# Kernel optimization log

Measured on AMD Instinct MI355X. Metric: run time of the kernel, lower is better.

## Reference

```python
import math
import jax, jax.numpy as jnp
import numpy as np

D_IN, R_S, T_MAX = 1024, 256, 2048
B, T = 8, 2048


def setup_inputs() -> dict:
    key = jax.random.key(0)
    ks = jax.random.split(key, 8)
    u = jax.random.normal(ks[0], (B, T, D_IN), dtype=jnp.float32)
    h0_r = jax.random.normal(ks[1], (B, R_S), dtype=jnp.float32)
    h0_i = jax.random.normal(ks[2], (B, R_S), dtype=jnp.float32)
    # parameters (lambda_raw randomized instead of zeros so sigmoid is nontrivial)
    lambda_raw = jax.random.normal(ks[3], (R_S,), dtype=jnp.float32)
    # omega init exactly as in the torch module
    log_min, log_max = math.log(1.0 / T_MAX), math.log(math.pi)
    n = np.arange(1, R_S + 1, dtype=np.float32)
    weyl_freqs = n * math.pi / R_S
    log_freqs = np.exp(np.linspace(log_min, log_max, R_S, dtype=np.float32))
    omega = jnp.asarray(0.5 * weyl_freqs + 0.5 * log_freqs, dtype=jnp.float32)
    W_proj = jax.random.normal(ks[4], (R_S, D_IN), dtype=jnp.float32) / math.sqrt(D_IN)
    W_res = jax.random.normal(ks[5], (2 * R_S, D_IN), dtype=jnp.float32) / math.sqrt(D_IN)
    ln_gamma = jnp.ones((2 * R_S,), dtype=jnp.float32)
    ln_beta = jnp.zeros((2 * R_S,), dtype=jnp.float32)
    return {"u": u, "h0_r": h0_r, "h0_i": h0_i, "lambda_raw": lambda_raw,
            "omega": omega, "W_proj": W_proj, "W_res": W_res,
            "ln_gamma": ln_gamma, "ln_beta": ln_beta}


def _layernorm(x, gamma, beta, eps=1e-5):
    mu = jnp.mean(x, axis=-1, keepdims=True)
    var = jnp.mean(jnp.square(x - mu), axis=-1, keepdims=True)
    return (x - mu) * jax.lax.rsqrt(var + eps) * gamma + beta


def reference(u, h0_r, h0_i, lambda_raw, omega, W_proj, W_res, ln_gamma, ln_beta):
    Bb, Tt, _ = u.shape
    lam = -jax.nn.sigmoid(lambda_raw) * 5.0                      # [R]
    t = jnp.arange(Tt, dtype=jnp.float32)                        # [T]
    decay = jnp.exp(lam[:, None] * t[None, :])                   # [R,T]
    phase = omega[:, None] * t[None, :]                          # [R,T]
    f_r = decay * jnp.cos(phase)
    f_i = decay * jnp.sin(phase)
    u_proj = jnp.einsum('btd,rd->brt', u, W_proj)                # [B,R,T]
    n_fft = 2 * Tt
    U_f = jnp.fft.rfft(u_proj, n=n_fft, axis=-1)                 # [B,R,F]
    F_r = jnp.fft.rfft(f_r, n=n_fft, axis=-1)[None]              # [1,R,F]
    F_i = jnp.fft.rfft(f_i, n=n_fft, axis=-1)[None]
    h_r = jnp.fft.irfft(U_f * F_r, n=n_fft, axis=-1)[..., :Tt]   # [B,R,T]
    h_i = jnp.fft.irfft(U_f * F_i, n=n_fft, axis=-1)[..., :Tt]
    # ZIR correction from initial state
    t_zir = t + 1.0
    decay_z = jnp.exp(lam[:, None] * t_zir[None, :])             # [R,T]
    phase_z = omega[:, None] * t_zir[None, :]
    f_r_z = decay_z * jnp.cos(phase_z)
    f_i_z = decay_z * jnp.sin(phase_z)
    h0r = h0_r[:, :, None]                                       # [B,R,1]
    h0i = h0_i[:, :, None]
    h_r = h_r + h0r * f_r_z[None] - h0i * f_i_z[None]
    h_i = h_i + h0r * f_i_z[None] + h0i * f_r_z[None]
    h_r = jnp.swapaxes(h_r, 1, 2)                                # [B,T,R]
    h_i = jnp.swapaxes(h_i, 1, 2)
    ssm_out = jnp.concatenate([h_r, h_i], axis=-1)               # [B,T,2R]
    res = jnp.einsum('btd,ed->bte', u, W_res)                    # [B,T,2R]
    out = _layernorm(ssm_out + res, ln_gamma, ln_beta)
    final_r = jax.lax.stop_gradient(h_r[:, -1])
    final_i = jax.lax.stop_gradient(h_i[:, -1])
    return out, final_r, final_i
```

## Files before the change

### kernel.cpp

```cpp
#include <hip/hip_runtime.h>
#include <math.h>

#define T_LEN 2048
#define BB    8
#define RS    256
#define DIN   1024
#define NE    768
#define M_TOT (BB * T_LEN)
#define LCH   32
#define NCH   (T_LEN / LCH)
#define OUT_MAIN (M_TOT * 512)

typedef unsigned short ushort;
typedef unsigned int   uint;
typedef short  short8  __attribute__((ext_vector_type(8)));
typedef float  f32x4   __attribute__((ext_vector_type(4)));
typedef ushort ushort8 __attribute__((ext_vector_type(8)));

__device__ __forceinline__ ushort f2bf_rn(float x) {
    uint u = __float_as_uint(x);
    return (ushort)((u + 0x7FFFu + ((u >> 16) & 1u)) >> 16);
}
__device__ __forceinline__ float bf2f(ushort b) {
    return __uint_as_float(((uint)b) << 16);
}

__device__ __forceinline__ void gload16(const ushort* g, ushort* l) {
    __builtin_amdgcn_global_load_lds(
        (const __attribute__((address_space(1))) uint*)g,
        (__attribute__((address_space(3))) uint*)l, 16, 0, 0);
}

__global__ __launch_bounds__(256) void split_kernel(
    const float* __restrict__ src, ushort* __restrict__ hi,
    ushort* __restrict__ lo, int n8)
{
    int i = blockIdx.x * blockDim.x + threadIdx.x;
    const int stride = gridDim.x * blockDim.x;
    for (; i < n8; i += stride) {
        const float4 x0 = ((const float4*)src)[(size_t)i * 2 + 0];
        const float4 x1 = ((const float4*)src)[(size_t)i * 2 + 1];
        const float xs[8] = {x0.x, x0.y, x0.z, x0.w, x1.x, x1.y, x1.z, x1.w};
        ushort8 hv, lv;
#pragma unroll
        for (int j = 0; j < 8; ++j) {
            const ushort hb = f2bf_rn(xs[j]);
            hv[j] = hb;
            lv[j] = f2bf_rn(xs[j] - bf2f(hb));
        }
        ((ushort8*)hi)[i] = hv;
        ((ushort8*)lo)[i] = lv;
    }
}

#define Bb 128
#define BK 32

__global__ __launch_bounds__(256) void gemm_mfma(
    const ushort* __restrict__ Uh, const ushort* __restrict__ Ul,
    const ushort* __restrict__ Wh, const ushort* __restrict__ Wl,
    float* __restrict__ C)
{
    __shared__ ushort Ah[Bb * BK], Al[Bb * BK], Bh[Bb * BK], Bl[Bb * BK];
    const int tid  = threadIdx.x;
    const int bn   = blockIdx.x;
    const int bm   = blockIdx.y;
    const int wid  = tid >> 6;
    const int lane = tid & 63;
    const int wr   = wid >> 1, wc = wid & 1;
    const int fr   = lane & 15;
    const int fq   = lane >> 4;

    const int srow = tid >> 2;
    const int skk  = (tid & 3) * 8;
    const ushort* gAh = Uh + (size_t)(bm * 128 + srow) * DIN + skk;
    const ushort* gAl = Ul + (size_t)(bm * 128 + srow) * DIN + skk;
    const ushort* gBh = Wh + (size_t)(bn * 128 + srow) * DIN + skk;
    const ushort* gBl = Wl + (size_t)(bn * 128 + srow) * DIN + skk;
    ushort* lAh0 = Ah + tid * 8; ushort* lAh1 = Ah + 64 * BK + tid * 8;
    ushort* lAl0 = Al + tid * 8; ushort* lAl1 = Al + 64 * BK + tid * 8;
    ushort* lBh0 = Bh + tid * 8; ushort* lBh1 = Bh + 64 * BK + tid * 8;
    ushort* lBl0 = Bl + tid * 8; ushort* lBl1 = Bl + 64 * BK + tid * 8;
    const size_t rstep = (size_t)64 * DIN;

    f32x4 acc[4][4];
#pragma unroll
    for (int m = 0; m < 4; ++m)
#pragma unroll
        for (int n = 0; n < 4; ++n) acc[m][n] = (f32x4){0.f, 0.f, 0.f, 0.f};

    for (int kk = 0; kk < DIN; kk += BK) {
        gload16(gAh + kk, lAh0); gload16(gAh + kk + rstep, lAh1);
        gload16(gAl + kk, lAl0); gload16(gAl + kk + rstep, lAl1);
        gload16(gBh + kk, lBh0); gload16(gBh + kk + rstep, lBh1);
        gload16(gBl + kk, lBl0); gload16(gBl + kk + rstep, lBl1);
        __syncthreads();

        short8 ah[4], al[4], bh[4], bl[4];
#pragma unroll
        for (int m = 0; m < 4; ++m) {
            const int row = wr * 64 + m * 16 + fr;
            ah[m] = *(const short8*)&Ah[row * BK + fq * 8];
            al[m] = *(const short8*)&Al[row * BK + fq * 8];
        }
#pragma unroll
        for (int n = 0; n < 4; ++n) {
            const int col = wc * 64 + n * 16 + fr;
            bh[n] = *(const short8*)&Bh[col * BK + fq * 8];
            bl[n] = *(const short8*)&Bl[col * BK + fq * 8];
        }
#pragma unroll
        for (int m = 0; m < 4; ++m)
#pragma unroll
            for (int n = 0; n < 4; ++n) {
                acc[m][n] = __builtin_amdgcn_mfma_f32_16x16x32_bf16(ah[m], bh[n], acc[m][n], 0, 0, 0);
                acc[m][n] = __builtin_amdgcn_mfma_f32_16x16x32_bf16(ah[m], bl[n], acc[m][n], 0, 0, 0);
                acc[m][n] = __builtin_amdgcn_mfma_f32_16x16x32_bf16(al[m], bh[n], acc[m][n], 0, 0, 0);
            }
        __syncthreads();
    }

    const int crow0 = bm * 128 + wr * 64;
    const int ccol0 = bn * 128 + wc * 64;
#pragma unroll
    for (int m = 0; m < 4; ++m) {
        const int row = crow0 + m * 16 + fq * 4;
#pragma unroll
        for (int n = 0; n < 4; ++n) {
            const int col = ccol0 + n * 16 + fr;
#pragma unroll
            for (int j = 0; j < 4; ++j)
                C[(size_t)(row + j) * NE + col] = acc[m][n][j];
        }
    }
}

__device__ inline void pole(const float* __restrict__ lraw, const float* __restrict__ om,
                            int r, float& zr, float& zi, float& lam, float& o)
{
    const float x   = lraw[r];
    const float sig = 1.f / (1.f + expf(-x));
    lam = -5.f * sig;
    o   = om[r];
    const float er = expf(lam);
    zr = er * cosf(o);
    zi = er * sinf(o);
}

__global__ __launch_bounds__(256) void carry_kernel(
    const float* __restrict__ C, const float* __restrict__ lraw,
    const float* __restrict__ om, float2* __restrict__ carry)
{
    const int c = blockIdx.x, b = blockIdx.y, r = threadIdx.x;
    __shared__ float tile[LCH][RS];
    const int m0 = b * T_LEN + c * LCH;
    for (int s = 0; s < LCH; ++s)
        tile[s][r] = C[(size_t)(m0 + s) * NE + r];
    float zr, zi, lam, o;
    pole(lraw, om, r, zr, zi, lam, o);
    __syncthreads();
    float hr = 0.f, hi = 0.f;
#pragma unroll 4
    for (int s = 0; s < LCH; ++s) {
        const float u  = tile[s][r];
        const float nr = zr * hr - zi * hi + u;
        const float ni = zr * hi + zi * hr;
        hr = nr; hi = ni;
    }
    carry[(size_t)(b * NCH + c) * RS + r] = make_float2(hr, hi);
}

__global__ __launch_bounds__(256) void chunk_scan_kernel(
    const float2* __restrict__ carry, const float* __restrict__ h0r,
    const float* __restrict__ h0i, const float* __restrict__ lraw,
    const float* __restrict__ om, float2* __restrict__ S, float* __restrict__ out)
{
    const int b = blockIdx.x, r = threadIdx.x;
    float zr, zi, lam, o;
    pole(lraw, om, r, zr, zi, lam, o);
    const float eL  = expf(lam * (float)LCH);
    const float zLr = eL * cosf(o * (float)LCH);
    const float zLi = eL * sinf(o * (float)LCH);
    float sr = h0r[b * RS + r];
    float si = h0i[b * RS + r];
    for (int c = 0; c < NCH; ++c) {
        S[(size_t)(b * NCH + c) * RS + r] = make_float2(sr, si);
        const float2 cc = carry[(size_t)(b * NCH + c) * RS + r];
        const float nr = zLr * sr - zLi * si + cc.x;
        const float ni = zLr * si + zLi * sr + cc.y;
        sr = nr; si = ni;
    }
    out[OUT_MAIN + b * RS + r]            = sr;
    out[OUT_MAIN + BB * RS + b * RS + r]  = si;
}

__global__ __launch_bounds__(256) void scan_ln_kernel(
    const float* __restrict__ C, const float2* __restrict__ S,
    const float* __restrict__ lraw, const float* __restrict__ om,
    const float* __restrict__ gamma, const float* __restrict__ beta,
    float* __restrict__ out)
{
    const int c = blockIdx.x, b = blockIdx.y, r = threadIdx.x;
    __shared__ float tile[LCH][RS];
    __shared__ float redA[4], redB[4];
    const int m0 = b * T_LEN + c * LCH;
    for (int s = 0; s < LCH; ++s)
        tile[s][r] = C[(size_t)(m0 + s) * NE + r];
    float zr, zi, lam, o;
    pole(lraw, om, r, zr, zi, lam, o);
    float2 st = S[(size_t)(b * NCH + c) * RS + r];
    const float g1 = gamma[r], g2 = gamma[RS + r];
    const float b1 = beta[r],  b2 = beta[RS + r];
    const int wid = r >> 6, lane = r & 63;
    __syncthreads();

    for (int s = 0; s < LCH; ++s) {
        const float u  = tile[s][r];
        const float hr = zr * st.x - zi * st.y + u;
        const float hi = zr * st.y + zi * st.x;
        st.x = hr; st.y = hi;
        const int m = m0 + s;
        const float x1 = hr + C[(size_t)m * NE + 256 + r];
        const float x2 = hi + C[(size_t)m * NE + 512 + r];
        float s1 = x1 + x2;
        float s2 = x1 * x1 + x2 * x2;
#pragma unroll
        for (int off = 1; off < 64; off <<= 1) {
            s1 += __shfl_xor(s1, off);
            s2 += __shfl_xor(s2, off);
        }
        if (lane == 0) { redA[wid] = s1; redB[wid] = s2; }
        __syncthreads();
        s1 = redA[0] + redA[1] + redA[2] + redA[3];
        s2 = redB[0] + redB[1] + redB[2] + redB[3];
        const float mu   = s1 * (1.f / 512.f);
        const float var  = s2 * (1.f / 512.f) - mu * mu;
        const float rstd = rsqrtf(var + 1e-5f);
        out[(size_t)m * 512 + r]       = (x1 - mu) * rstd * g1 + b1;
        out[(size_t)m * 512 + 256 + r] = (x2 - mu) * rstd * g2 + b2;
        __syncthreads();
    }
}

extern "C" void kernel_launch(void* const* d_in, const int* in_sizes, int n_in,
                              void* d_out, int out_size, void* d_ws, size_t ws_size,
                              hipStream_t stream)
{
    const float* u    = (const float*)d_in[0];
    const float* h0r  = (const float*)d_in[1];
    const float* h0i  = (const float*)d_in[2];
    const float* lraw = (const float*)d_in[3];
    const float* omg  = (const float*)d_in[4];
    const float* Wp   = (const float*)d_in[5];
    const float* Wr   = (const float*)d_in[6];
    const float* gam  = (const float*)d_in[7];
    const float* bet  = (const float*)d_in[8];
    float* out = (float*)d_out;

    float*  C     = (float*)d_ws;
    float2* carry = (float2*)(C + (size_t)M_TOT * NE);
    float2* S     = carry + (size_t)BB * NCH * RS;
    ushort* Uhi   = (ushort*)(S + (size_t)BB * NCH * RS);
    ushort* Ulo   = Uhi + (size_t)M_TOT * DIN;
    ushort* Whi   = Ulo + (size_t)M_TOT * DIN;
    ushort* Wlo   = Whi + (size_t)NE * DIN;

    split_kernel<<<2048, 256, 0, stream>>>(u, Uhi, Ulo, M_TOT * DIN / 8);
    split_kernel<<<128, 256, 0, stream>>>(Wp, Whi, Wlo, RS * DIN / 8);
    split_kernel<<<128, 256, 0, stream>>>(Wr, Whi + (size_t)RS * DIN,
                                          Wlo + (size_t)RS * DIN, 2 * RS * DIN / 8);

    gemm_mfma<<<dim3(NE / 128, M_TOT / 128), 256, 0, stream>>>(Uhi, Ulo, Whi, Wlo, C);

    carry_kernel<<<dim3(NCH, BB), 256, 0, stream>>>(C, lraw, omg, carry);
    chunk_scan_kernel<<<BB, 256, 0, stream>>>(carry, h0r, h0i, lraw, omg, S, out);
    scan_ln_kernel<<<dim3(NCH, BB), 256, 0, stream>>>(C, (const float2*)S, lraw, omg, gam, bet, out);
}
```

Before: 256.5 us.

## Double-buffer GEMM with 32x32 MFMA, fuse split kernels, restructure scan and layernorm

The GEMM now uses 32x32x16 bf16 MFMA with a k-blocked LDS layout and double-buffered global-to-LDS loads. This is meant to overlap memory with compute, and a block-id swizzle is added for L2 locality. The three split launches are merged into one. The carry kernel reads C directly instead of staging it through LDS. The chunk scan stages carries in LDS, and the scan+layernorm kernel batches 8 timesteps so that one wave normalizes a full row with vector loads and stores. The layernorm restructure removes the per-step block barriers, at the cost of more LDS use and register pressure in the GEMM.

```diff
diff --git a/kernel.cpp b/kernel.cpp
--- a/kernel.cpp
+++ b/kernel.cpp
@@ -14,7 +14,7 @@
 typedef unsigned short ushort;
 typedef unsigned int   uint;
 typedef short  short8  __attribute__((ext_vector_type(8)));
-typedef float  f32x4   __attribute__((ext_vector_type(4)));
+typedef float  f32x16  __attribute__((ext_vector_type(16)));
 typedef ushort ushort8 __attribute__((ext_vector_type(8)));
 
 __device__ __forceinline__ ushort f2bf_rn(float x) {
@@ -31,108 +31,132 @@
         (__attribute__((address_space(3))) uint*)l, 16, 0, 0);
 }
 
+#define N8U  (M_TOT * DIN / 8)
+#define N8WP (RS * DIN / 8)
+#define N8WR (2 * RS * DIN / 8)
+#define N8TOT (N8U + N8WP + N8WR)
+
 __global__ __launch_bounds__(256) void split_kernel(
-    const float* __restrict__ src, ushort* __restrict__ hi,
-    ushort* __restrict__ lo, int n8)
-{
-    int i = blockIdx.x * blockDim.x + threadIdx.x;
-    const int stride = gridDim.x * blockDim.x;
-    for (; i < n8; i += stride) {
-        const float4 x0 = ((const float4*)src)[(size_t)i * 2 + 0];
-        const float4 x1 = ((const float4*)src)[(size_t)i * 2 + 1];
-        const float xs[8] = {x0.x, x0.y, x0.z, x0.w, x1.x, x1.y, x1.z, x1.w};
-        ushort8 hv, lv;
-#pragma unroll
-        for (int j = 0; j < 8; ++j) {
-            const ushort hb = f2bf_rn(xs[j]);
-            hv[j] = hb;
-            lv[j] = f2bf_rn(xs[j] - bf2f(hb));
-        }
-        ((ushort8*)hi)[i] = hv;
-        ((ushort8*)lo)[i] = lv;
-    }
-}
-
-#define Bb 128
-#define BK 32
+    const float* __restrict__ u, const float* __restrict__ wp,
+    const float* __restrict__ wr, ushort* __restrict__ Uhi,
+    ushort* __restrict__ Ulo, ushort* __restrict__ Whi, ushort* __restrict__ Wlo)
+{
+    const int i = blockIdx.x * 256 + threadIdx.x;
+    if (i >= N8TOT) return;
+    const float* src; ushort* hi; ushort* lo; int j;
+    if (i < N8U)              { src = u;  hi = Uhi; lo = Ulo; j = i; }
+    else if (i < N8U + N8WP)  { src = wp; hi = Whi; lo = Wlo; j = i - N8U; }
+    else                      { src = wr; hi = Whi + (size_t)RS * DIN;
+                                lo = Wlo + (size_t)RS * DIN; j = i - N8U - N8WP; }
+    const float4 x0 = ((const float4*)src)[(size_t)j * 2 + 0];
+    const float4 x1 = ((const float4*)src)[(size_t)j * 2 + 1];
+    const float xs[8] = {x0.x, x0.y, x0.z, x0.w, x1.x, x1.y, x1.z, x1.w};
+    ushort8 hv, lv;
+#pragma unroll
+    for (int k = 0; k < 8; ++k) {
+        const ushort hb = f2bf_rn(xs[k]);
+        hv[k] = hb;
+        lv[k] = f2bf_rn(xs[k] - bf2f(hb));
+    }
+    ((ushort8*)hi)[j] = hv;
+    ((ushort8*)lo)[j] = lv;
+}
+
+#define BKK 32
+#define KTILES (DIN / BKK)
 
 __global__ __launch_bounds__(256) void gemm_mfma(
     const ushort* __restrict__ Uh, const ushort* __restrict__ Ul,
     const ushort* __restrict__ Wh, const ushort* __restrict__ Wl,
     float* __restrict__ C)
 {
-    __shared__ ushort Ah[Bb * BK], Al[Bb * BK], Bh[Bb * BK], Bl[Bb * BK];
+    __shared__ ushort lds[2][4][4096];
     const int tid  = threadIdx.x;
-    const int bn   = blockIdx.x;
-    const int bm   = blockIdx.y;
+    const int id   = blockIdx.x;
+    const int sid  = (id & 7) * 96 + (id >> 3);
+    const int bn   = sid % 6;
+    const int bm   = sid / 6;
     const int wid  = tid >> 6;
     const int lane = tid & 63;
     const int wr   = wid >> 1, wc = wid & 1;
-    const int fr   = lane & 15;
-    const int fq   = lane >> 4;
-
-    const int srow = tid >> 2;
-    const int skk  = (tid & 3) * 8;
-    const ushort* gAh = Uh + (size_t)(bm * 128 + srow) * DIN + skk;
-    const ushort* gAl = Ul + (size_t)(bm * 128 + srow) * DIN + skk;
-    const ushort* gBh = Wh + (size_t)(bn * 128 + srow) * DIN + skk;
-    const ushort* gBl = Wl + (size_t)(bn * 128 + srow) * DIN + skk;
-    ushort* lAh0 = Ah + tid * 8; ushort* lAh1 = Ah + 64 * BK + tid * 8;
-    ushort* lAl0 = Al + tid * 8; ushort* lAl1 = Al + 64 * BK + tid * 8;
-    ushort* lBh0 = Bh + tid * 8; ushort* lBh1 = Bh + 64 * BK + tid * 8;
-    ushort* lBl0 = Bl + tid * 8; ushort* lBl1 = Bl + 64 * BK + tid * 8;
-    const size_t rstep = (size_t)64 * DIN;
-
-    f32x4 acc[4][4];
-#pragma unroll
-    for (int m = 0; m < 4; ++m)
-#pragma unroll
-        for (int n = 0; n < 4; ++n) acc[m][n] = (f32x4){0.f, 0.f, 0.f, 0.f};
-
-    for (int kk = 0; kk < DIN; kk += BK) {
-        gload16(gAh + kk, lAh0); gload16(gAh + kk + rstep, lAh1);
-        gload16(gAl + kk, lAl0); gload16(gAl + kk + rstep, lAl1);
-        gload16(gBh + kk, lBh0); gload16(gBh + kk + rstep, lBh1);
-        gload16(gBl + kk, lBl0); gload16(gBl + kk + rstep, lBl1);
-        __syncthreads();
-
-        short8 ah[4], al[4], bh[4], bl[4];
-#pragma unroll
-        for (int m = 0; m < 4; ++m) {
-            const int row = wr * 64 + m * 16 + fr;
-            ah[m] = *(const short8*)&Ah[row * BK + fq * 8];
-            al[m] = *(const short8*)&Al[row * BK + fq * 8];
-        }
-#pragma unroll
-        for (int n = 0; n < 4; ++n) {
-            const int col = wc * 64 + n * 16 + fr;
-            bh[n] = *(const short8*)&Bh[col * BK + fq * 8];
-            bl[n] = *(const short8*)&Bl[col * BK + fq * 8];
-        }
-#pragma unroll
-        for (int m = 0; m < 4; ++m)
-#pragma unroll
-            for (int n = 0; n < 4; ++n) {
-                acc[m][n] = __builtin_amdgcn_mfma_f32_16x16x32_bf16(ah[m], bh[n], acc[m][n], 0, 0, 0);
-                acc[m][n] = __builtin_amdgcn_mfma_f32_16x16x32_bf16(ah[m], bl[n], acc[m][n], 0, 0, 0);
-                acc[m][n] = __builtin_amdgcn_mfma_f32_16x16x32_bf16(al[m], bh[n], acc[m][n], 0, 0, 0);
-            }
-        __syncthreads();
+    const int l31  = lane & 31;
+    const int lh   = lane >> 5;
+
+    const int srow = tid & 127;
+    const int kb0  = tid >> 7;
+    const size_t arow = (size_t)(bm * 128 + srow) * DIN + kb0 * 8;
+    const size_t brow = (size_t)(bn * 128 + srow) * DIN + kb0 * 8;
+    const ushort* gsrc[4] = { Uh + arow, Ul + arow, Wh + brow, Wl + brow };
+    const int lslot0 = tid * 8;
+    const int lslot1 = (256 + tid) * 8;
+
+    f32x16 acc[2][2];
+#pragma unroll
+    for (int m = 0; m < 2; ++m)
+#pragma unroll
+        for (int n = 0; n < 2; ++n)
+#pragma unroll
+            for (int j = 0; j < 16; ++j) acc[m][n][j] = 0.f;
+
+#pragma unroll
+    for (int p = 0; p < 4; ++p) {
+        gload16(gsrc[p],      &lds[0][p][lslot0]);
+        gload16(gsrc[p] + 16, &lds[0][p][lslot1]);
+    }
+    __syncthreads();
+
+    int bufc = 0;
+    for (int kt = 0; kt < KTILES; ++kt) {
+        const int kk = kt * BKK;
+        if (kt + 1 < KTILES) {
+#pragma unroll
+            for (int p = 0; p < 4; ++p) {
+                gload16(gsrc[p] + kk + BKK,      &lds[bufc ^ 1][p][lslot0]);
+                gload16(gsrc[p] + kk + BKK + 16, &lds[bufc ^ 1][p][lslot1]);
+            }
+        }
+#pragma unroll
+        for (int t2 = 0; t2 < 2; ++t2) {
+            const int kblk = t2 * 2 + lh;
+            short8 ah[2], al[2], bh[2], bl[2];
+#pragma unroll
+            for (int m = 0; m < 2; ++m) {
+                const int row = wr * 64 + m * 32 + l31;
+                ah[m] = *(const short8*)&lds[bufc][0][kblk * 1024 + row * 8];
+                al[m] = *(const short8*)&lds[bufc][1][kblk * 1024 + row * 8];
+            }
+#pragma unroll
+            for (int n = 0; n < 2; ++n) {
+                const int col = wc * 64 + n * 32 + l31;
+                bh[n] = *(const short8*)&lds[bufc][2][kblk * 1024 + col * 8];
+                bl[n] = *(const short8*)&lds[bufc][3][kblk * 1024 + col * 8];
+            }
+#pragma unroll
+            for (int m = 0; m < 2; ++m)
+#pragma unroll
+                for (int n = 0; n < 2; ++n) {
+                    acc[m][n] = __builtin_amdgcn_mfma_f32_32x32x16_bf16(ah[m], bh[n], acc[m][n], 0, 0, 0);
+                    acc[m][n] = __builtin_amdgcn_mfma_f32_32x32x16_bf16(ah[m], bl[n], acc[m][n], 0, 0, 0);
+                    acc[m][n] = __builtin_amdgcn_mfma_f32_32x32x16_bf16(al[m], bh[n], acc[m][n], 0, 0, 0);
+                }
+        }
+        __syncthreads();
+        bufc ^= 1;
     }
 
     const int crow0 = bm * 128 + wr * 64;
-    const int ccol0 = bn * 128 + wc * 64;
-#pragma unroll
-    for (int m = 0; m < 4; ++m) {
-        const int row = crow0 + m * 16 + fq * 4;
-#pragma unroll
-        for (int n = 0; n < 4; ++n) {
-            const int col = ccol0 + n * 16 + fr;
-#pragma unroll
-            for (int j = 0; j < 4; ++j)
-                C[(size_t)(row + j) * NE + col] = acc[m][n][j];
-        }
-    }
+    const int ccol0 = bn * 128 + wc * 64 + l31;
+#pragma unroll
+    for (int m = 0; m < 2; ++m)
+#pragma unroll
+        for (int n = 0; n < 2; ++n) {
+            const int col = ccol0 + n * 32;
+#pragma unroll
+            for (int j = 0; j < 16; ++j) {
+                const int row = crow0 + m * 32 + (j & 3) + 8 * (j >> 2) + 4 * lh;
+                C[(size_t)row * NE + col] = acc[m][n][j];
+            }
+        }
 }
 
 __device__ inline void pole(const float* __restrict__ lraw, const float* __restrict__ om,
@@ -152,17 +176,14 @@
     const float* __restrict__ om, float2* __restrict__ carry)
 {
     const int c = blockIdx.x, b = blockIdx.y, r = threadIdx.x;
-    __shared__ float tile[LCH][RS];
     const int m0 = b * T_LEN + c * LCH;
-    for (int s = 0; s < LCH; ++s)
-        tile[s][r] = C[(size_t)(m0 + s) * NE + r];
     float zr, zi, lam, o;
     pole(lraw, om, r, zr, zi, lam, o);
-    __syncthreads();
+    const float* p = C + (size_t)m0 * NE + r;
     float hr = 0.f, hi = 0.f;
-#pragma unroll 4
+#pragma unroll 8
     for (int s = 0; s < LCH; ++s) {
-        const float u  = tile[s][r];
+        const float u  = p[(size_t)s * NE];
         const float nr = zr * hr - zi * hi + u;
         const float ni = zr * hi + zi * hr;
         hr = nr; hi = ni;
@@ -176,6 +197,7 @@
     const float* __restrict__ om, float2* __restrict__ S, float* __restrict__ out)
 {
     const int b = blockIdx.x, r = threadIdx.x;
+    __shared__ float2 cs[32 * RS];
     float zr, zi, lam, o;
     pole(lraw, om, r, zr, zi, lam, o);
     const float eL  = expf(lam * (float)LCH);
@@ -183,15 +205,23 @@
     const float zLi = eL * sinf(o * (float)LCH);
     float sr = h0r[b * RS + r];
     float si = h0i[b * RS + r];
-    for (int c = 0; c < NCH; ++c) {
-        S[(size_t)(b * NCH + c) * RS + r] = make_float2(sr, si);
-        const float2 cc = carry[(size_t)(b * NCH + c) * RS + r];
-        const float nr = zLr * sr - zLi * si + cc.x;
-        const float ni = zLr * si + zLi * sr + cc.y;
-        sr = nr; si = ni;
-    }
-    out[OUT_MAIN + b * RS + r]            = sr;
-    out[OUT_MAIN + BB * RS + b * RS + r]  = si;
+    for (int half = 0; half < 2; ++half) {
+        __syncthreads();
+        const float4* src = (const float4*)(carry + ((size_t)b * NCH + half * 32) * RS);
+        float4* dst = (float4*)cs;
+        for (int i = r; i < 32 * RS / 2; i += 256) dst[i] = src[i];
+        __syncthreads();
+        for (int cc = 0; cc < 32; ++cc) {
+            const int c = half * 32 + cc;
+            S[((size_t)b * NCH + c) * RS + r] = make_float2(sr, si);
+            const float2 k = cs[cc * RS + r];
+            const float nr = zLr * sr - zLi * si + k.x;
+            const float ni = zLr * si + zLi * sr + k.y;
+            sr = nr; si = ni;
+        }
+    }
+    out[OUT_MAIN + b * RS + r]           = sr;
+    out[OUT_MAIN + BB * RS + b * RS + r] = si;
 }
 
 __global__ __launch_bounds__(256) void scan_ln_kernel(
@@ -201,43 +231,59 @@
     float* __restrict__ out)
 {
     const int c = blockIdx.x, b = blockIdx.y, r = threadIdx.x;
-    __shared__ float tile[LCH][RS];
-    __shared__ float redA[4], redB[4];
+    __shared__ float xt[8][512];
     const int m0 = b * T_LEN + c * LCH;
-    for (int s = 0; s < LCH; ++s)
-        tile[s][r] = C[(size_t)(m0 + s) * NE + r];
     float zr, zi, lam, o;
     pole(lraw, om, r, zr, zi, lam, o);
     float2 st = S[(size_t)(b * NCH + c) * RS + r];
-    const float g1 = gamma[r], g2 = gamma[RS + r];
-    const float b1 = beta[r],  b2 = beta[RS + r];
     const int wid = r >> 6, lane = r & 63;
-    __syncthreads();
-
-    for (int s = 0; s < LCH; ++s) {
-        const float u  = tile[s][r];
-        const float hr = zr * st.x - zi * st.y + u;
-        const float hi = zr * st.y + zi * st.x;
-        st.x = hr; st.y = hi;
-        const int m = m0 + s;
-        const float x1 = hr + C[(size_t)m * NE + 256 + r];
-        const float x2 = hi + C[(size_t)m * NE + 512 + r];
-        float s1 = x1 + x2;
-        float s2 = x1 * x1 + x2 * x2;
-#pragma unroll
-        for (int off = 1; off < 64; off <<= 1) {
-            s1 += __shfl_xor(s1, off);
-            s2 += __shfl_xor(s2, off);
-        }
-        if (lane == 0) { redA[wid] = s1; redB[wid] = s2; }
-        __syncthreads();
-        s1 = redA[0] + redA[1] + redA[2] + redA[3];
-        s2 = redB[0] + redB[1] + redB[2] + redB[3];
-        const float mu   = s1 * (1.f / 512.f);
-        const float var  = s2 * (1.f / 512.f) - mu * mu;
-        const float rstd = rsqrtf(var + 1e-5f);
-        out[(size_t)m * 512 + r]       = (x1 - mu) * rstd * g1 + b1;
-        out[(size_t)m * 512 + 256 + r] = (x2 - mu) * rstd * g2 + b2;
+    const float4 g0  = *(const float4*)&gamma[lane * 8];
+    const float4 g1  = *(const float4*)&gamma[lane * 8 + 4];
+    const float4 be0 = *(const float4*)&beta[lane * 8];
+    const float4 be1 = *(const float4*)&beta[lane * 8 + 4];
+
+    for (int batch = 0; batch < 4; ++batch) {
+        const int s0 = batch * 8;
+#pragma unroll
+        for (int s = 0; s < 8; ++s) {
+            const int m = m0 + s0 + s;
+            const float u  = C[(size_t)m * NE + r];
+            const float hr = zr * st.x - zi * st.y + u;
+            const float hi = zr * st.y + zi * st.x;
+            st.x = hr; st.y = hi;
+            xt[s][r]       = hr + C[(size_t)m * NE + 256 + r];
+            xt[s][256 + r] = hi + C[(size_t)m * NE + 512 + r];
+        }
+        __syncthreads();
+#pragma unroll
+        for (int rr = 0; rr < 2; ++rr) {
+            const int s = wid * 2 + rr;
+            const int m = m0 + s0 + s;
+            const float4 x0 = *(const float4*)&xt[s][lane * 8];
+            const float4 x1 = *(const float4*)&xt[s][lane * 8 + 4];
+            float s1 = (x0.x + x0.y) + (x0.z + x0.w) + (x1.x + x1.y) + (x1.z + x1.w);
+            float s2 = (x0.x * x0.x + x0.y * x0.y) + (x0.z * x0.z + x0.w * x0.w)
+                     + (x1.x * x1.x + x1.y * x1.y) + (x1.z * x1.z + x1.w * x1.w);
+#pragma unroll
+            for (int off = 1; off < 64; off <<= 1) {
+                s1 += __shfl_xor(s1, off);
+                s2 += __shfl_xor(s2, off);
+            }
+            const float mu   = s1 * (1.f / 512.f);
+            const float var  = s2 * (1.f / 512.f) - mu * mu;
+            const float rstd = rsqrtf(var + 1e-5f);
+            float4 o0, o1;
+            o0.x = (x0.x - mu) * rstd * g0.x + be0.x;
+            o0.y = (x0.y - mu) * rstd * g0.y + be0.y;
+            o0.z = (x0.z - mu) * rstd * g0.z + be0.z;
+            o0.w = (x0.w - mu) * rstd * g0.w + be0.w;
+            o1.x = (x1.x - mu) * rstd * g1.x + be1.x;
+            o1.y = (x1.y - mu) * rstd * g1.y + be1.y;
+            o1.z = (x1.z - mu) * rstd * g1.z + be1.z;
+            o1.w = (x1.w - mu) * rstd * g1.w + be1.w;
+            *(float4*)&out[(size_t)m * 512 + lane * 8]     = o0;
+            *(float4*)&out[(size_t)m * 512 + lane * 8 + 4] = o1;
+        }
         __syncthreads();
     }
 }
@@ -265,13 +311,8 @@
     ushort* Whi   = Ulo + (size_t)M_TOT * DIN;
     ushort* Wlo   = Whi + (size_t)NE * DIN;
 
-    split_kernel<<<2048, 256, 0, stream>>>(u, Uhi, Ulo, M_TOT * DIN / 8);
-    split_kernel<<<128, 256, 0, stream>>>(Wp, Whi, Wlo, RS * DIN / 8);
-    split_kernel<<<128, 256, 0, stream>>>(Wr, Whi + (size_t)RS * DIN,
-                                          Wlo + (size_t)RS * DIN, 2 * RS * DIN / 8);
-
-    gemm_mfma<<<dim3(NE / 128, M_TOT / 128), 256, 0, stream>>>(Uhi, Ulo, Whi, Wlo, C);
-
+    split_kernel<<<N8TOT / 256, 256, 0, stream>>>(u, Wp, Wr, Uhi, Ulo, Whi, Wlo);
+    gemm_mfma<<<768, 256, 0, stream>>>(Uhi, Ulo, Whi, Wlo, C);
     carry_kernel<<<dim3(NCH, BB), 256, 0, stream>>>(C, lraw, omg, carry);
     chunk_scan_kernel<<<BB, 256, 0, stream>>>(carry, h0r, h0i, lraw, omg, S, out);
     scan_ln_kernel<<<dim3(NCH, BB), 256, 0, stream>>>(C, (const float2*)S, lraw, omg, gam, bet, out);
```

New measurement: 262.8 us. +2.4%, slower.
